# Performance work log

Measured on AMD Instinct MI355X. Metric: run time of the kernel, lower is better.

Reference implementation:

```python
import jax, jax.numpy as jnp
import numpy as np

E = 8          # num experts
H = 1024       # hidden size
I = 512        # moe intermediate size
K = 2          # top_k
B, S = 1, 2048


def setup_inputs() -> dict:
    key = jax.random.key(0)
    k1, k2, k3, k4, k5 = jax.random.split(key, 5)
    hidden_states = jax.random.normal(k1, (B, S, H), dtype=jnp.float32)
    router_indices = jax.random.randint(k2, (B * S, K), 0, E, dtype=jnp.int64)
    routing_weights = jax.random.uniform(k3, (B * S, K), dtype=jnp.float32)
    # kaiming-uniform-ish init per expert
    bound_gu = 1.0 / np.sqrt(H)
    bound_d = 1.0 / np.sqrt(I)
    gate_up_proj = jax.random.uniform(k4, (E, H, 2 * I), dtype=jnp.float32,
                                      minval=-bound_gu, maxval=bound_gu)
    down_proj = jax.random.uniform(k5, (E, I, H), dtype=jnp.float32,
                                   minval=-bound_d, maxval=bound_d)
    return {
        "hidden_states": hidden_states,
        "router_indices": router_indices,
        "routing_weights": routing_weights,
        "gate_up_proj": gate_up_proj,
        "down_proj": down_proj,
    }


def reference(hidden_states, router_indices, routing_weights, gate_up_proj, down_proj):
    b, s, h = hidden_states.shape
    x = hidden_states.reshape(b * s, h)                    # [T, H]
    # combine weights: sum over top-k slots of routing weight for each expert
    one_hot = jax.nn.one_hot(router_indices, E, dtype=x.dtype)   # [T, K, E]
    combine = jnp.einsum('tke,tk->te', one_hot, routing_weights)  # [T, E]
    # dense dispatch: every token through every expert, masked/weighted by combine
    gate_up = jnp.einsum('th,ehf->tef', x, gate_up_proj)   # [T, E, 2I]
    gate, up = jnp.split(gate_up, 2, axis=-1)              # [T, E, I] each
    inter = jax.nn.silu(gate) * up                         # SwiGLU (no limit clamp)
    out = jnp.einsum('tef,efh,te->th', inter, down_proj, combine)  # [T, H]
    return out.reshape(b, s, h)
```

## Files before the change

kernel.cpp:

```cpp
#include <hip/hip_runtime.h>
#include <stdint.h>

#define T_TOK 2048
#define H_DIM 1024
#define ID    512
#define E_NUM 8
#define NPAIR 4096
#define BM    64
#define MAXTILES 72

typedef _Float16 half_t;
typedef _Float16 f16x8 __attribute__((ext_vector_type(8)));
typedef _Float16 f16x4 __attribute__((ext_vector_type(4)));
typedef float    f32x4 __attribute__((ext_vector_type(4)));

#define XB_OFF      ((size_t)0)
#define WGU_OFF     ((size_t)(4u << 20))
#define WDN_OFF     ((size_t)(20u << 20))
#define INTER_OFF   ((size_t)(28u << 20))
#define META_OFF    ((size_t)(32u << 20))
#define PAIRW_OFF   ((size_t)((32u << 20) + 65536))
#define CONTRIB_OFF ((size_t)(36u << 20))

__device__ __forceinline__ void gload_lds16(const void* g, void* l) {
    __builtin_amdgcn_global_load_lds(
        (const __attribute__((address_space(1))) unsigned int*)g,
        (__attribute__((address_space(3))) unsigned int*)l,
        16, 0, 0);
}

template <int NT>
__device__ __forceinline__ void cvt_tile64(const float* __restrict__ in,
                                           half_t* __restrict__ out,
                                           int r0, int c0, int out_stride,
                                           char* smem) {
    float (*tile)[65] = (float(*)[65])smem;
    int tid = threadIdx.x;
#pragma unroll
    for (int it = 0; it < 1024 / NT; it++) {
        int idx = tid + it * NT;
        int r = idx >> 4, c4 = (idx & 15) * 4;
        float4 v = *(const float4*)(in + (size_t)(r0 + r) * 1024 + c0 + c4);
        tile[r][c4] = v.x; tile[r][c4 + 1] = v.y; tile[r][c4 + 2] = v.z; tile[r][c4 + 3] = v.w;
    }
    __syncthreads();
#pragma unroll
    for (int it = 0; it < 1024 / NT; it++) {
        int idx = tid + it * NT;
        int oc = idx >> 4, r4 = (idx & 15) * 4;
        f16x4 o;
        o[0] = (half_t)tile[r4][oc];
        o[1] = (half_t)tile[r4 + 1][oc];
        o[2] = (half_t)tile[r4 + 2][oc];
        o[3] = (half_t)tile[r4 + 3][oc];
        *(f16x4*)(out + (size_t)(c0 + oc) * out_stride + r0 + r4) = o;
    }
}

__global__ __launch_bounds__(256) void k_prep(const float* __restrict__ x,
                                              const int* __restrict__ ridx,
                                              const float* __restrict__ rw,
                                              const float* __restrict__ wgu,
                                              half_t* __restrict__ xb,
                                              half_t* __restrict__ wguT,
                                              int* __restrict__ meta,
                                              float* __restrict__ pair_w) {
    __shared__ char smem[16704];
    int b = blockIdx.x, tid = threadIdx.x;
    if (b < 1024) {
        int g = b * 256 + tid;
        size_t b0 = (size_t)g * 8;
        float4 v0 = *(const float4*)(x + b0);
        float4 v1 = *(const float4*)(x + b0 + 4);
        f16x8 o;
        o[0] = (half_t)v0.x; o[1] = (half_t)v0.y; o[2] = (half_t)v0.z; o[3] = (half_t)v0.w;
        o[4] = (half_t)v1.x; o[5] = (half_t)v1.y; o[6] = (half_t)v1.z; o[7] = (half_t)v1.w;
        *(f16x8*)(xb + b0) = o;
    } else if (b == 1024) {
        __shared__ int cnt[E_NUM], cur[E_NUM], base[E_NUM];
        if (tid < E_NUM) { cnt[tid] = 0; cur[tid] = 0; }
        __syncthreads();
        for (int i = tid; i < NPAIR; i += 256) atomicAdd(&cnt[ridx[i]], 1);
        __syncthreads();
        if (tid == 0) {
            int acc = 0, nt = 0;
            for (int e = 0; e < E_NUM; e++) {
                base[e] = acc;
                for (int r = 0; r < cnt[e]; r += BM) {
                    meta[8 + nt] = e; meta[88 + nt] = acc + r; meta[168 + nt] = acc + cnt[e]; nt++;
                }
                acc += cnt[e];
            }
            meta[0] = nt;
        }
        __syncthreads();
        for (int i = tid; i < NPAIR; i += 256) {
            int e = ridx[i];
            int pos = atomicAdd(&cur[e], 1);
            int slot = base[e] + pos;
            meta[256 + slot] = i >> 1;
            meta[256 + NPAIR + i] = slot;
            pair_w[slot] = rw[i];
        }
    } else {
        int t = b - 1025;
        int e = t >> 8, rem = t & 255;
        int h0 = (rem >> 4) * 64, f0 = (rem & 15) * 64;
        cvt_tile64<256>(wgu + (size_t)e * 1024 * 1024, wguT + (size_t)e * 1024 * 1024,
                        h0, f0, 1024, smem);
    }
}

template <int MODE>
__global__ __launch_bounds__(256) void k_gemm(const int* __restrict__ meta,
                                              const half_t* __restrict__ amat,
                                              const half_t* __restrict__ wT,
                                              const float* __restrict__ pair_w,
                                              void* __restrict__ outp,
                                              const float* __restrict__ aux_in,
                                              half_t* __restrict__ aux_out) {
    constexpr int KSZ = MODE ? ID : H_DIM;
    constexpr int NKT = KSZ / 64;
    __shared__ __align__(16) char smem[49152];

    int d = blockIdx.x;
    if (MODE == 0 && d >= 576) {
        int d2 = d - 576;
        int e = d2 >> 7, rem = d2 & 127;
        int h0 = (rem >> 3) * 64, i0 = (rem & 7) * 64;
        cvt_tile64<256>(aux_in + (size_t)e * ID * 1024, aux_out + (size_t)e * 1024 * ID,
                        i0, h0, ID, smem);
        return;
    }

    int l = (d & 7) * MAXTILES + (d >> 3);
    int bx = l >> 3, by = l & 7;
    int nt = meta[0];
    if (bx >= nt) return;
    int e = meta[8 + bx], row0 = meta[88 + bx], rend = meta[168 + bx];
    const int* pair_token = meta + 256;

    int tid = threadIdx.x, lane = tid & 63, wid = tid >> 6;

    const half_t* asrc[2]; int aoff[2];
#pragma unroll
    for (int i = 0; i < 2; i++) {
        int gch = wid * 2 + i, c = gch * 64 + lane;
        int r = c >> 3, pc = c & 7, lc = pc ^ (r & 7);
        int pr = row0 + r; if (pr > NPAIR - 1) pr = NPAIR - 1;
        const half_t* rowp = (MODE == 0) ? amat + (size_t)pair_token[pr] * KSZ
                                         : amat + (size_t)pr * KSZ;
        asrc[i] = rowp + lc * 8;
        aoff[i] = gch * 1024 + lane * 16;
    }
    const half_t* wbase = wT + (size_t)e * 1024 * KSZ;
    const half_t* bsrc[4]; int boff[4];
#pragma unroll
    for (int i = 0; i < 4; i++) {
        int gch = wid * 4 + i, c = gch * 64 + lane;
        int r = c >> 3, pc = c & 7, lc = pc ^ (r & 7);
        int physcol;
        if (MODE == 0) {
            int wn_r = r >> 5, fn_r = (r >> 4) & 1, ll = r & 15;
            physcol = by * 64 + wn_r * 16 + ll + (fn_r ? 512 : 0);
        } else {
            physcol = by * 128 + r;
        }
        bsrc[i] = wbase + (size_t)physcol * KSZ + lc * 8;
        boff[i] = gch * 1024 + lane * 16;
    }

#define STAGE(buf, kt)                                                             \
    {                                                                              \
        _Pragma("unroll")                                                          \
        for (int i = 0; i < 2; i++)                                                \
            gload_lds16(asrc[i] + (kt) * 64, smem + (buf) * 8192 + aoff[i]);       \
        _Pragma("unroll")                                                          \
        for (int i = 0; i < 4; i++)                                                \
            gload_lds16(bsrc[i] + (kt) * 64, smem + 16384 + (buf) * 16384 + boff[i]); \
    }

    f32x4 acc[4][2] = {};

    STAGE(0, 0);
    __syncthreads();

    for (int kt = 0; kt < NKT; kt++) {
        int cur = kt & 1;
        if (kt + 1 < NKT) STAGE(cur ^ 1, kt + 1);
        const char* Ab = smem + cur * 8192;
        const char* Bb = smem + 16384 + cur * 16384;
#pragma unroll
        for (int ks = 0; ks < 2; ks++) {
            f16x8 af[4], bf2[2];
#pragma unroll
            for (int f = 0; f < 4; f++) {
                int ar = f * 16 + (lane & 15);
                int apc = (ks * 4 + (lane >> 4)) ^ (ar & 7);
                af[f] = *(const f16x8*)(Ab + ar * 128 + apc * 16);
            }
#pragma unroll
            for (int f = 0; f < 2; f++) {
                int br = wid * 32 + f * 16 + (lane & 15);
                int bpc = (ks * 4 + (lane >> 4)) ^ (br & 7);
                bf2[f] = *(const f16x8*)(Bb + br * 128 + bpc * 16);
            }
#pragma unroll
            for (int fm = 0; fm < 4; fm++)
#pragma unroll
                for (int fn = 0; fn < 2; fn++)
                    acc[fm][fn] = __builtin_amdgcn_mfma_f32_16x16x32_f16(af[fm], bf2[fn], acc[fm][fn], 0, 0, 0);
        }
        __syncthreads();
    }

    if (MODE == 0) {
        half_t* inter = (half_t*)outp;
#pragma unroll
        for (int fm = 0; fm < 4; fm++) {
            int rbase = fm * 16 + (lane >> 4) * 4;
#pragma unroll
            for (int j = 0; j < 4; j++) {
                int packed = row0 + rbase + j;
                if (packed < rend) {
                    float gv = acc[fm][0][j], uv = acc[fm][1][j];
                    float s = gv / (1.0f + __expf(-gv)) * uv;
                    int col = by * 64 + wid * 16 + (lane & 15);
                    inter[(size_t)packed * ID + col] = (half_t)s;
                }
            }
        }
    } else {
        half_t* contrib = (half_t*)outp;
#pragma unroll
        for (int fm = 0; fm < 4; fm++) {
            int rbase = fm * 16 + (lane >> 4) * 4;
#pragma unroll
            for (int j = 0; j < 4; j++) {
                int packed = row0 + rbase + j;
                if (packed < rend) {
                    float pw = pair_w[packed];
#pragma unroll
                    for (int fn = 0; fn < 2; fn++) {
                        int col = by * 128 + wid * 32 + fn * 16 + (lane & 15);
                        contrib[(size_t)packed * H_DIM + col] = (half_t)(acc[fm][fn][j] * pw);
                    }
                }
            }
        }
    }
#undef STAGE
}

__global__ __launch_bounds__(256) void k_gather(const half_t* __restrict__ contrib,
                                                const int* __restrict__ meta,
                                                float* __restrict__ out) {
    int t = blockIdx.x, c4 = threadIdx.x * 4;
    const int* slot_of = meta + 256 + NPAIR;
    int s0 = slot_of[2 * t], s1 = slot_of[2 * t + 1];
    f16x4 a = *(const f16x4*)(contrib + (size_t)s0 * H_DIM + c4);
    f16x4 b = *(const f16x4*)(contrib + (size_t)s1 * H_DIM + c4);
    float4 o;
    o.x = (float)a[0] + (float)b[0];
    o.y = (float)a[1] + (float)b[1];
    o.z = (float)a[2] + (float)b[2];
    o.w = (float)a[3] + (float)b[3];
    *(float4*)(out + (size_t)t * H_DIM + c4) = o;
}

extern "C" void kernel_launch(void* const* d_in, const int* in_sizes, int n_in,
                              void* d_out, int out_size, void* d_ws, size_t ws_size,
                              hipStream_t stream) {
    const float* x    = (const float*)d_in[0];
    const int*   ridx = (const int*)d_in[1];
    const float* rw   = (const float*)d_in[2];
    const float* wgu  = (const float*)d_in[3];
    const float* wdn  = (const float*)d_in[4];
    float* out = (float*)d_out;

    char* ws = (char*)d_ws;
    half_t* xb      = (half_t*)(ws + XB_OFF);
    half_t* wguT    = (half_t*)(ws + WGU_OFF);
    half_t* wdnT    = (half_t*)(ws + WDN_OFF);
    half_t* inter   = (half_t*)(ws + INTER_OFF);
    int*    meta    = (int*)(ws + META_OFF);
    float*  pair_w  = (float*)(ws + PAIRW_OFF);
    half_t* contrib = (half_t*)(ws + CONTRIB_OFF);

    k_prep<<<3073, 256, 0, stream>>>(x, ridx, rw, wgu, xb, wguT, meta, pair_w);
    k_gemm<0><<<1600, 256, 0, stream>>>(meta, xb, wguT, pair_w, inter, wdn, wdnT);
    k_gemm<1><<<576, 256, 0, stream>>>(meta, inter, wdnT, pair_w, contrib, nullptr, nullptr);
    k_gather<<<T_TOK, 256, 0, stream>>>(contrib, meta, out);
}
```

Before: 59.73 us.

## Fuse fp32 weight transpose-convert into GEMM B-tile loading

Removes the separate passes that transposed and converted both weight tensors to fp16 in workspace. Each GEMM now reads fp32 weights directly into registers, converts them to fp16 and writes them swizzled into LDS, with the global load for the next tile issued before the current tile's MFMAs. This avoids writing and re-reading 24MB of fp16 weights and shrinks the prep and first GEMM grids. In exchange, each expert's fp32 weights are read by every token tile that uses it, which doubles per-tile B bytes and adds conversion work and register pressure inside the GEMM loop.

Result: slower. 74.52 us (+24.7%).

```diff
diff --git a/kernel.cpp b/kernel.cpp
--- a/kernel.cpp
+++ b/kernel.cpp
@@ -15,12 +15,10 @@
 typedef float    f32x4 __attribute__((ext_vector_type(4)));
 
 #define XB_OFF      ((size_t)0)
-#define WGU_OFF     ((size_t)(4u << 20))
-#define WDN_OFF     ((size_t)(20u << 20))
-#define INTER_OFF   ((size_t)(28u << 20))
-#define META_OFF    ((size_t)(32u << 20))
-#define PAIRW_OFF   ((size_t)((32u << 20) + 65536))
-#define CONTRIB_OFF ((size_t)(36u << 20))
+#define INTER_OFF   ((size_t)(4u << 20))
+#define META_OFF    ((size_t)(8u << 20))
+#define PAIRW_OFF   ((size_t)((8u << 20) + 65536))
+#define CONTRIB_OFF ((size_t)(12u << 20))
 
 __device__ __forceinline__ void gload_lds16(const void* g, void* l) {
     __builtin_amdgcn_global_load_lds(
@@ -29,43 +27,12 @@
         16, 0, 0);
 }
 
-template <int NT>
-__device__ __forceinline__ void cvt_tile64(const float* __restrict__ in,
-                                           half_t* __restrict__ out,
-                                           int r0, int c0, int out_stride,
-                                           char* smem) {
-    float (*tile)[65] = (float(*)[65])smem;
-    int tid = threadIdx.x;
-#pragma unroll
-    for (int it = 0; it < 1024 / NT; it++) {
-        int idx = tid + it * NT;
-        int r = idx >> 4, c4 = (idx & 15) * 4;
-        float4 v = *(const float4*)(in + (size_t)(r0 + r) * 1024 + c0 + c4);
-        tile[r][c4] = v.x; tile[r][c4 + 1] = v.y; tile[r][c4 + 2] = v.z; tile[r][c4 + 3] = v.w;
-    }
-    __syncthreads();
-#pragma unroll
-    for (int it = 0; it < 1024 / NT; it++) {
-        int idx = tid + it * NT;
-        int oc = idx >> 4, r4 = (idx & 15) * 4;
-        f16x4 o;
-        o[0] = (half_t)tile[r4][oc];
-        o[1] = (half_t)tile[r4 + 1][oc];
-        o[2] = (half_t)tile[r4 + 2][oc];
-        o[3] = (half_t)tile[r4 + 3][oc];
-        *(f16x4*)(out + (size_t)(c0 + oc) * out_stride + r0 + r4) = o;
-    }
-}
-
 __global__ __launch_bounds__(256) void k_prep(const float* __restrict__ x,
                                               const int* __restrict__ ridx,
                                               const float* __restrict__ rw,
-                                              const float* __restrict__ wgu,
                                               half_t* __restrict__ xb,
-                                              half_t* __restrict__ wguT,
                                               int* __restrict__ meta,
                                               float* __restrict__ pair_w) {
-    __shared__ char smem[16704];
     int b = blockIdx.x, tid = threadIdx.x;
     if (b < 1024) {
         int g = b * 256 + tid;
@@ -76,7 +43,7 @@
         o[0] = (half_t)v0.x; o[1] = (half_t)v0.y; o[2] = (half_t)v0.z; o[3] = (half_t)v0.w;
         o[4] = (half_t)v1.x; o[5] = (half_t)v1.y; o[6] = (half_t)v1.z; o[7] = (half_t)v1.w;
         *(f16x8*)(xb + b0) = o;
-    } else if (b == 1024) {
+    } else {
         __shared__ int cnt[E_NUM], cur[E_NUM], base[E_NUM];
         if (tid < E_NUM) { cnt[tid] = 0; cur[tid] = 0; }
         __syncthreads();
@@ -102,37 +69,20 @@
             meta[256 + NPAIR + i] = slot;
             pair_w[slot] = rw[i];
         }
-    } else {
-        int t = b - 1025;
-        int e = t >> 8, rem = t & 255;
-        int h0 = (rem >> 4) * 64, f0 = (rem & 15) * 64;
-        cvt_tile64<256>(wgu + (size_t)e * 1024 * 1024, wguT + (size_t)e * 1024 * 1024,
-                        h0, f0, 1024, smem);
     }
 }
 
 template <int MODE>
 __global__ __launch_bounds__(256) void k_gemm(const int* __restrict__ meta,
                                               const half_t* __restrict__ amat,
-                                              const half_t* __restrict__ wT,
+                                              const float* __restrict__ w32,
                                               const float* __restrict__ pair_w,
-                                              void* __restrict__ outp,
-                                              const float* __restrict__ aux_in,
-                                              half_t* __restrict__ aux_out) {
+                                              void* __restrict__ outp) {
     constexpr int KSZ = MODE ? ID : H_DIM;
     constexpr int NKT = KSZ / 64;
     __shared__ __align__(16) char smem[49152];
 
     int d = blockIdx.x;
-    if (MODE == 0 && d >= 576) {
-        int d2 = d - 576;
-        int e = d2 >> 7, rem = d2 & 127;
-        int h0 = (rem >> 3) * 64, i0 = (rem & 7) * 64;
-        cvt_tile64<256>(aux_in + (size_t)e * ID * 1024, aux_out + (size_t)e * 1024 * ID,
-                        i0, h0, ID, smem);
-        return;
-    }
-
     int l = (d & 7) * MAXTILES + (d >> 3);
     int bx = l >> 3, by = l & 7;
     int nt = meta[0];
@@ -153,43 +103,46 @@
         asrc[i] = rowp + lc * 8;
         aoff[i] = gch * 1024 + lane * 16;
     }
-    const half_t* wbase = wT + (size_t)e * 1024 * KSZ;
-    const half_t* bsrc[4]; int boff[4];
-#pragma unroll
-    for (int i = 0; i < 4; i++) {
-        int gch = wid * 4 + i, c = gch * 64 + lane;
-        int r = c >> 3, pc = c & 7, lc = pc ^ (r & 7);
-        int physcol;
-        if (MODE == 0) {
-            int wn_r = r >> 5, fn_r = (r >> 4) & 1, ll = r & 15;
-            physcol = by * 64 + wn_r * 16 + ll + (fn_r ? 512 : 0);
-        } else {
-            physcol = by * 128 + r;
-        }
-        bsrc[i] = wbase + (size_t)physcol * KSZ + lc * 8;
-        boff[i] = gch * 1024 + lane * 16;
-    }
-
-#define STAGE(buf, kt)                                                             \
-    {                                                                              \
-        _Pragma("unroll")                                                          \
-        for (int i = 0; i < 2; i++)                                                \
-            gload_lds16(asrc[i] + (kt) * 64, smem + (buf) * 8192 + aoff[i]);       \
-        _Pragma("unroll")                                                          \
-        for (int i = 0; i < 4; i++)                                                \
-            gload_lds16(bsrc[i] + (kt) * 64, smem + 16384 + (buf) * 16384 + boff[i]); \
-    }
+
+    int br0 = 4 * (lane & 31);
+    int cchunk = 2 * wid + (lane >> 5);
+    int physcol0;
+    if (MODE == 0) {
+        int wn_r = br0 >> 5, fn_r = (br0 >> 4) & 1, ll = br0 & 15;
+        physcol0 = by * 64 + wn_r * 16 + ll + (fn_r ? 512 : 0);
+    } else {
+        physcol0 = by * 128 + br0;
+    }
+    const float* wsrc = w32 + (size_t)e * KSZ * 1024 + physcol0;
+
+    f32x4 ld[8];
+    auto loadB = [&](int kt) {
+        const float* p = wsrc + (size_t)(kt * 64 + cchunk * 8) * 1024;
+#pragma unroll
+        for (int j = 0; j < 8; j++) ld[j] = *(const f32x4*)(p + (size_t)j * 1024);
+    };
+    auto writeB = [&](int buf) {
+        char* bb = smem + 16384 + buf * 16384;
+#pragma unroll
+        for (int i = 0; i < 4; i++) {
+            int br = br0 + i;
+            f16x8 v;
+#pragma unroll
+            for (int j = 0; j < 8; j++) v[j] = (half_t)ld[j][i];
+            *(f16x8*)(bb + br * 128 + (cchunk ^ (br & 7)) * 16) = v;
+        }
+    };
+    auto stageA = [&](int buf, int kt) {
+#pragma unroll
+        for (int i = 0; i < 2; i++)
+            gload_lds16(asrc[i] + kt * 64, smem + buf * 8192 + aoff[i]);
+    };
 
     f32x4 acc[4][2] = {};
 
-    STAGE(0, 0);
-    __syncthreads();
-
-    for (int kt = 0; kt < NKT; kt++) {
-        int cur = kt & 1;
-        if (kt + 1 < NKT) STAGE(cur ^ 1, kt + 1);
-        const char* Ab = smem + cur * 8192;
-        const char* Bb = smem + 16384 + cur * 16384;
+    auto compute = [&](int buf) {
+        const char* Ab = smem + buf * 8192;
+        const char* Bb = smem + 16384 + buf * 16384;
 #pragma unroll
         for (int ks = 0; ks < 2; ks++) {
             f16x8 af[4], bf2[2];
@@ -211,6 +164,18 @@
                 for (int fn = 0; fn < 2; fn++)
                     acc[fm][fn] = __builtin_amdgcn_mfma_f32_16x16x32_f16(af[fm], bf2[fn], acc[fm][fn], 0, 0, 0);
         }
+    };
+
+    loadB(0);
+    stageA(0, 0);
+    writeB(0);
+    __syncthreads();
+
+    for (int kt = 0; kt < NKT; kt++) {
+        int cur = kt & 1;
+        if (kt + 1 < NKT) { loadB(kt + 1); stageA(cur ^ 1, kt + 1); }
+        compute(cur);
+        if (kt + 1 < NKT) writeB(cur ^ 1);
         __syncthreads();
     }
 
@@ -249,7 +214,6 @@
             }
         }
     }
-#undef STAGE
 }
 
 __global__ __launch_bounds__(256) void k_gather(const half_t* __restrict__ contrib,
@@ -280,15 +244,13 @@
 
     char* ws = (char*)d_ws;
     half_t* xb      = (half_t*)(ws + XB_OFF);
-    half_t* wguT    = (half_t*)(ws + WGU_OFF);
-    half_t* wdnT    = (half_t*)(ws + WDN_OFF);
     half_t* inter   = (half_t*)(ws + INTER_OFF);
     int*    meta    = (int*)(ws + META_OFF);
     float*  pair_w  = (float*)(ws + PAIRW_OFF);
     half_t* contrib = (half_t*)(ws + CONTRIB_OFF);
 
-    k_prep<<<3073, 256, 0, stream>>>(x, ridx, rw, wgu, xb, wguT, meta, pair_w);
-    k_gemm<0><<<1600, 256, 0, stream>>>(meta, xb, wguT, pair_w, inter, wdn, wdnT);
-    k_gemm<1><<<576, 256, 0, stream>>>(meta, inter, wdnT, pair_w, contrib, nullptr, nullptr);
+    k_prep<<<1025, 256, 0, stream>>>(x, ridx, rw, xb, meta, pair_w);
+    k_gemm<0><<<576, 256, 0, stream>>>(meta, xb, wgu, pair_w, inter);
+    k_gemm<1><<<576, 256, 0, stream>>>(meta, inter, wdn, pair_w, contrib);
     k_gather<<<T_TOK, 256, 0, stream>>>(contrib, meta, out);
 }
```
